# Kernel optimization log

Hardware: AMD Instinct MI355X
Metric: run time of the kernel (lower is better)

Reference implementation:

```python
import jax, jax.numpy as jnp
import numpy as np

B, H, K, D = 4096, 3, 32768, 128


def setup_inputs() -> dict:
    key = jax.random.key(0)
    k_in, k_emb = jax.random.split(key)
    inputs = jax.random.normal(k_in, (B, 1, D), dtype=jnp.float32)
    # xavier-uniform-ish init with per-head decay 0.5**h (gain 6.0), as in the module
    ks = jax.random.split(k_emb, H)
    tables = []
    for h in range(H):
        gain = 6.0 * (0.5 ** h)
        bound = gain * np.sqrt(6.0 / (K + D))
        tables.append(jax.random.uniform(ks[h], (K, D), jnp.float32, -bound, bound))
    emb = jnp.stack(tables, axis=0)  # [H, K, D]
    return {"inputs": inputs, "emb": emb}


def reference(inputs, emb):
    # Eval-mode HRQ forward: per-head negative squared-L2 distances to the
    # codebook on the running residual, hard argmax assignment, summed codes.
    x = inputs[:, 0, :]                      # [B, D]
    n_heads = emb.shape[0]
    resid = x
    quantized = jnp.zeros_like(x)
    codes = []
    for h in range(n_heads):
        W = emb[h]                            # [K, D]
        # -(||r||^2 + ||w||^2 - 2 r.w)  -> argmax == nearest code
        dists = -(jnp.sum(resid * resid, axis=1, keepdims=True)
                  + jnp.sum(W * W, axis=1)
                  - 2.0 * resid @ W.T)        # [B, K]
        c = jnp.argmax(dists, axis=-1)        # [B]
        q = jnp.take(W, c, axis=0)            # onehot(c) @ W == gather
        resid = resid - q
        quantized = quantized + q
        codes.append(c)
    loss = jnp.zeros(x.shape[0], dtype=inputs.dtype)
    return loss, quantized.reshape(inputs.shape), jnp.stack(codes, axis=1)
```

## Files before the change

### kernel.cpp

```cpp
#include <hip/hip_runtime.h>
#include <math.h>

#define NB 4096
#define NH 3
#define NK 32768
#define ND 128
#define KA 256
#define KB 256
#define RB 64
#define CS 16
#define CPB (NK / CS)
#define CI 128
#define NCI (CPB / CI)

typedef _Float16 half8_t __attribute__((ext_vector_type(8)));
typedef _Float16 half2_t __attribute__((ext_vector_type(2)));
typedef float f32x4 __attribute__((ext_vector_type(4)));
typedef __attribute__((address_space(1))) const unsigned int gu32_t;
typedef __attribute__((address_space(3))) unsigned int lu32_t;

__global__ __launch_bounds__(64) void init_kernel(const float* __restrict__ inp,
                                                  float* __restrict__ resid,
                                                  float* __restrict__ rr,
                                                  float* __restrict__ out,
                                                  _Float16* __restrict__ Aext) {
  int row = blockIdx.x;
  int lane = threadIdx.x;
  const float2* ip = (const float2*)(inp + row * ND);
  float2 v = ip[lane];
  ((float2*)(resid + row * ND))[lane] = v;
  ((float2*)(out + NB + row * ND))[lane] = make_float2(0.f, 0.f);
  if (lane == 0) out[row] = 0.f;
  _Float16 h0 = (_Float16)v.x, h1 = (_Float16)v.y;
  _Float16 l0 = (_Float16)(v.x - (float)h0), l1 = (_Float16)(v.y - (float)h1);
  half2_t h = {h0, h1}, l = {l0, l1};
  _Float16* base = Aext + (size_t)row * KA;
  *(half2_t*)(base + 2 * lane) = h;
  *(half2_t*)(base + 128 + 2 * lane) = l;
  float s = v.x * v.x + v.y * v.y;
  #pragma unroll
  for (int m = 32; m; m >>= 1) s += __shfl_xor(s, m, 64);
  if (lane == 0) rr[row] = s;
}

__global__ __launch_bounds__(256) void norms_kernel(const float* __restrict__ emb,
                                                    float* __restrict__ norms) {
  int row = blockIdx.x * 4 + (threadIdx.x >> 6);
  int lane = threadIdx.x & 63;
  const float2* wp = (const float2*)(emb + (size_t)row * ND);
  float2 v = wp[lane];
  float s = v.x * v.x + v.y * v.y;
  #pragma unroll
  for (int m = 32; m; m >>= 1) s += __shfl_xor(s, m, 64);
  if (lane == 0) norms[row] = s;
}

__global__ __launch_bounds__(256) void split_w_all_kernel(const float* __restrict__ emb,
                                                          _Float16* __restrict__ Bext) {
  const int head = blockIdx.x >> 11;
  const int cg = blockIdx.x & 2047;
  const int n_lo = threadIdx.x & 15;
  const int c = threadIdx.x >> 4;
  const int n = cg * 16 + n_lo;

  const float4* wp = (const float4*)(emb + (size_t)head * NK * ND + (size_t)n * ND + c * 8);
  float4 v0 = wp[0], v1 = wp[1];
  float xv[8] = {v0.x, v0.y, v0.z, v0.w, v1.x, v1.y, v1.z, v1.w};
  half8_t h, l;
  #pragma unroll
  for (int j = 0; j < 8; ++j) {
    _Float16 hh = (_Float16)xv[j];
    h[j] = hh;
    l[j] = (_Float16)(xv[j] - (float)hh);
  }
  const int ks0 = c >> 2;
  const int klo = c & 3;
  _Float16* base = Bext + (size_t)head * NK * KB + (size_t)(cg >> 2) * 16384 +
                   (cg & 3) * 512 + klo * 128 + n_lo * 8;
  *(half8_t*)(base + ks0 * 2048) = h;
  *(half8_t*)(base + (4 + ks0) * 2048) = l;
}

__global__ __launch_bounds__(256, 2) void score_mfma_kernel(
    const _Float16* __restrict__ Aext, const _Float16* __restrict__ Bext,
    const float* __restrict__ rr, const float* __restrict__ normh,
    float* __restrict__ partial_s, int* __restrict__ partial_i) {
  __shared__ __align__(16) _Float16 Ash[RB * KA];
  __shared__ __align__(16) float rrsh[RB];

  const int bid = blockIdx.x;
  const int cs = bid & (CS - 1);
  const int rowb = bid >> 4;
  const int rowBase = rowb * RB;
  const int colBase0 = cs * CPB;

  const int tid = threadIdx.x;
  const int lane = tid & 63;
  const int wn = tid >> 6;
  const int l15 = lane & 15;
  const int q = lane >> 4;

  {
    const int mrow = lane >> 3;
    const int cg = (lane & 7) ^ (mrow & 7);
    #pragma unroll
    for (int i = 0; i < 8; ++i) {
      int wc = wn * 8 + i;
      int p = wc >> 3;
      int m0 = (wc & 7) * 8;
      const _Float16* gA = Aext + (size_t)(rowBase + m0 + mrow) * KA + p * 64 + cg * 8;
      __builtin_amdgcn_global_load_lds((gu32_t*)gA, (lu32_t*)&Ash[(p * 64 + m0) * 64], 16, 0, 0);
    }
  }
  if (tid < RB) rrsh[tid] = rr[rowBase + tid];

  int aaddr0[4];
  #pragma unroll
  for (int mt = 0; mt < 4; ++mt) {
    int m = mt * 16 + l15;
    int slot = q ^ (m & 7);
    aaddr0[mt] = (m * 8 + slot) * 16;
  }

  float bs[16];
  int bi[16];
  #pragma unroll
  for (int t = 0; t < 16; ++t) { bs[t] = -INFINITY; bi[t] = 0x7fffffff; }

  unsigned bo = (unsigned)((colBase0 + (NCI - 1) * CI + wn * 32) >> 6) * 16384u +
                (((unsigned)(colBase0 + (NCI - 1) * CI + wn * 32) >> 4) & 3u) * 512u +
                (unsigned)lane * 8u;
  half8_t bh[2], bl[2];
  #pragma unroll
  for (int tn = 0; tn < 2; ++tn) {
    bh[tn] = *(const half8_t*)(Bext + bo + (unsigned)(tn * 512));
    bl[tn] = *(const half8_t*)(Bext + bo + (unsigned)(8192 + tn * 512));
  }

  __syncthreads();

  const f32x4 Z = {0.f, 0.f, 0.f, 0.f};

  #pragma unroll 1
  for (int ci = NCI - 1; ci >= 0; --ci) {
    const int ncol = colBase0 + ci * CI + wn * 32;
    const int ci_n = (ci > 0) ? ci - 1 : 0;
    const int ncol_n = colBase0 + ci_n * CI + wn * 32;
    const unsigned bon = (unsigned)(ncol_n >> 6) * 16384u +
                         (((unsigned)ncol_n >> 4) & 3u) * 512u + (unsigned)lane * 8u;

    float nw[2];
    #pragma unroll
    for (int tn = 0; tn < 2; ++tn) nw[tn] = normh[ncol + tn * 16 + l15];

    f32x4 acc[4][2];
    half8_t nh[2], nl[2];

    {
      #pragma unroll
      for (int tn = 0; tn < 2; ++tn) {
        nh[tn] = *(const half8_t*)(Bext + bo + (unsigned)(2048 + tn * 512));
        nl[tn] = *(const half8_t*)(Bext + bo + (unsigned)(2048 + 8192 + tn * 512));
      }
      __builtin_amdgcn_s_setprio(1);
      #pragma unroll
      for (int mt = 0; mt < 4; ++mt) {
        half8_t ah = *(const half8_t*)((const char*)Ash + aaddr0[mt]);
        half8_t al = *(const half8_t*)((const char*)Ash + aaddr0[mt] + 16384);
        acc[mt][0] = __builtin_amdgcn_mfma_f32_16x16x32_f16(ah, bh[0], Z, 0, 0, 0);
        acc[mt][1] = __builtin_amdgcn_mfma_f32_16x16x32_f16(ah, bh[1], Z, 0, 0, 0);
        acc[mt][0] = __builtin_amdgcn_mfma_f32_16x16x32_f16(al, bh[0], acc[mt][0], 0, 0, 0);
        acc[mt][1] = __builtin_amdgcn_mfma_f32_16x16x32_f16(al, bh[1], acc[mt][1], 0, 0, 0);
        acc[mt][0] = __builtin_amdgcn_mfma_f32_16x16x32_f16(ah, bl[0], acc[mt][0], 0, 0, 0);
        acc[mt][1] = __builtin_amdgcn_mfma_f32_16x16x32_f16(ah, bl[1], acc[mt][1], 0, 0, 0);
      }
      __builtin_amdgcn_s_setprio(0);
      bh[0] = nh[0]; bh[1] = nh[1];
      bl[0] = nl[0]; bl[1] = nl[1];
    }

    #pragma unroll
    for (int kc = 1; kc < 4; ++kc) {
      const unsigned po = (kc < 3) ? bo + (unsigned)((kc + 1) * 2048) : bon;
      #pragma unroll
      for (int tn = 0; tn < 2; ++tn) {
        nh[tn] = *(const half8_t*)(Bext + po + (unsigned)(tn * 512));
        nl[tn] = *(const half8_t*)(Bext + po + (unsigned)(8192 + tn * 512));
      }
      const int axor = (kc & 1) << 6;
      const int abase = (kc >> 1) * 8192;
      __builtin_amdgcn_s_setprio(1);
      #pragma unroll
      for (int mt = 0; mt < 4; ++mt) {
        half8_t ah = *(const half8_t*)((const char*)Ash + ((aaddr0[mt] ^ axor) + abase));
        half8_t al = *(const half8_t*)((const char*)Ash + ((aaddr0[mt] ^ axor) + abase + 16384));
        acc[mt][0] = __builtin_amdgcn_mfma_f32_16x16x32_f16(ah, bh[0], acc[mt][0], 0, 0, 0);
        acc[mt][1] = __builtin_amdgcn_mfma_f32_16x16x32_f16(ah, bh[1], acc[mt][1], 0, 0, 0);
        acc[mt][0] = __builtin_amdgcn_mfma_f32_16x16x32_f16(al, bh[0], acc[mt][0], 0, 0, 0);
        acc[mt][1] = __builtin_amdgcn_mfma_f32_16x16x32_f16(al, bh[1], acc[mt][1], 0, 0, 0);
        acc[mt][0] = __builtin_amdgcn_mfma_f32_16x16x32_f16(ah, bl[0], acc[mt][0], 0, 0, 0);
        acc[mt][1] = __builtin_amdgcn_mfma_f32_16x16x32_f16(ah, bl[1], acc[mt][1], 0, 0, 0);
      }
      __builtin_amdgcn_s_setprio(0);
      bh[0] = nh[0]; bh[1] = nh[1];
      bl[0] = nl[0]; bl[1] = nl[1];
    }

    #pragma unroll
    for (int tn = 1; tn >= 0; --tn) {
      const float nwv = nw[tn];
      const int cidx = ncol + tn * 16 + l15;
      #pragma unroll
      for (int mt = 0; mt < 4; ++mt) {
        const f32x4 rvv = *(const f32x4*)&rrsh[mt * 16 + q * 4];
        #pragma unroll
        for (int reg = 0; reg < 4; ++reg) {
          const int s = mt * 4 + reg;
          float t1 = rvv[reg] + nwv;
          float v = fmaf(2.0f, acc[mt][tn][reg], -t1);
          if (v >= bs[s]) { bs[s] = v; bi[s] = cidx; }
        }
      }
    }
    bo = bon;
  }

  __syncthreads();
  float* red_s = (float*)Ash;
  int* red_i = (int*)Ash + RB * 4;
  #pragma unroll
  for (int t = 0; t < 16; ++t) {
    float s = bs[t];
    int ii = bi[t];
    #pragma unroll
    for (int mask = 1; mask <= 8; mask <<= 1) {
      float os = __shfl_xor(s, mask, 64);
      int oi = __shfl_xor(ii, mask, 64);
      if (os > s || (os == s && oi < ii)) { s = os; ii = oi; }
    }
    if (l15 == 0) {
      int rloc = (t >> 2) * 16 + q * 4 + (t & 3);
      red_s[rloc * 4 + wn] = s;
      red_i[rloc * 4 + wn] = ii;
    }
  }
  __syncthreads();
  if (tid < RB) {
    float s0 = red_s[tid * 4];
    int i0 = red_i[tid * 4];
    #pragma unroll
    for (int x = 1; x < 4; ++x) {
      float sx = red_s[tid * 4 + x];
      int ix = red_i[tid * 4 + x];
      if (sx > s0 || (sx == s0 && ix < i0)) { s0 = sx; i0 = ix; }
    }
    partial_s[(size_t)(rowBase + tid) * CS + cs] = s0;
    partial_i[(size_t)(rowBase + tid) * CS + cs] = i0;
  }
}

__global__ __launch_bounds__(64) void reduce_update_kernel(const float* __restrict__ embh,
                                                           float* __restrict__ resid,
                                                           float* __restrict__ rr,
                                                           const float* __restrict__ ps,
                                                           const int* __restrict__ pi,
                                                           float* __restrict__ out,
                                                           _Float16* __restrict__ Aext, int h) {
  int row = blockIdx.x;
  int lane = threadIdx.x;
  float bs = -INFINITY;
  int bi = 0x7fffffff;
  if (lane < CS) {
    bs = ps[(size_t)row * CS + lane];
    bi = pi[(size_t)row * CS + lane];
  }
  #pragma unroll
  for (int m = 8; m; m >>= 1) {
    float os = __shfl_xor(bs, m, 64);
    int oi = __shfl_xor(bi, m, 64);
    if (os > bs || (os == bs && oi < bi)) { bs = os; bi = oi; }
  }
  int c = __shfl(bi, 0, 64);
  if (lane == 0) out[NB + NB * ND + row * NH + h] = (float)c;

  const float* wv = embh + (size_t)c * ND;
  float q0 = wv[lane], q1 = wv[lane + 64];
  float r0 = resid[row * ND + lane] - q0;
  float r1 = resid[row * ND + lane + 64] - q1;
  resid[row * ND + lane] = r0;
  resid[row * ND + lane + 64] = r1;
  out[NB + row * ND + lane] += q0;
  out[NB + row * ND + lane + 64] += q1;

  _Float16 h0 = (_Float16)r0, l0 = (_Float16)(r0 - (float)h0);
  _Float16 h1 = (_Float16)r1, l1 = (_Float16)(r1 - (float)h1);
  _Float16* ab = Aext + (size_t)row * KA;
  ab[lane] = h0;       ab[lane + 64] = h1;
  ab[128 + lane] = l0; ab[128 + lane + 64] = l1;

  float s = r0 * r0 + r1 * r1;
  #pragma unroll
  for (int m = 32; m; m >>= 1) s += __shfl_xor(s, m, 64);
  if (lane == 0) rr[row] = s;
}

extern "C" void kernel_launch(void* const* d_in, const int* in_sizes, int n_in,
                              void* d_out, int out_size, void* d_ws, size_t ws_size,
                              hipStream_t stream) {
  const float* inp = (const float*)d_in[0];
  const float* emb = (const float*)d_in[1];
  float* out = (float*)d_out;

  float* resid = (float*)d_ws;
  float* rr = resid + NB * ND;
  float* norms = rr + NB;
  float* ps = norms + NH * NK;
  int* pi = (int*)(ps + (size_t)NB * CS);
  _Float16* Aext = (_Float16*)(pi + (size_t)NB * CS);
  _Float16* Bext = Aext + (size_t)NB * KA;

  hipLaunchKernelGGL(init_kernel, dim3(NB), dim3(64), 0, stream, inp, resid, rr, out, Aext);
  hipLaunchKernelGGL(norms_kernel, dim3(NH * NK / 4), dim3(256), 0, stream, emb, norms);
  hipLaunchKernelGGL(split_w_all_kernel, dim3(NH * NK / 16), dim3(256), 0, stream, emb, Bext);
  for (int h = 0; h < NH; ++h) {
    hipLaunchKernelGGL(score_mfma_kernel, dim3((NB / RB) * CS), dim3(256), 0, stream,
                       Aext, Bext + (size_t)h * NK * KB, rr, norms + (size_t)h * NK, ps, pi);
    hipLaunchKernelGGL(reduce_update_kernel, dim3(NB), dim3(64), 0, stream,
                       emb + (size_t)h * NK * ND, resid, rr, ps, pi, out, Aext, h);
  }
}
```

Before: 423.2 us.

## Double row tile to 128 with 8 waves sharing B loads, pack argmax indices

Doubles the row block per workgroup to 128 and uses 8 waves (two row halves by four column groups), so each fetched B codebook tile is reused across twice as many rows and global B traffic is halved. The per-lane best-index registers are replaced by packed 8-bit chunk/tile tags that are decoded into column indices only at the end, which saves registers for the higher launch-bounds occupancy target. The risks are a larger LDS footprint, more register pressure under launch_bounds(512,4), and half as many workgroups.

```diff
diff --git a/kernel.cpp b/kernel.cpp
--- a/kernel.cpp
+++ b/kernel.cpp
@@ -7,7 +7,7 @@
 #define ND 128
 #define KA 256
 #define KB 256
-#define RB 64
+#define RB 128
 #define CS 16
 #define CPB (NK / CS)
 #define CI 128
@@ -81,7 +81,7 @@
   *(half8_t*)(base + (4 + ks0) * 2048) = l;
 }
 
-__global__ __launch_bounds__(256, 2) void score_mfma_kernel(
+__global__ __launch_bounds__(512, 4) void score_mfma_kernel(
     const _Float16* __restrict__ Aext, const _Float16* __restrict__ Bext,
     const float* __restrict__ rr, const float* __restrict__ normh,
     float* __restrict__ partial_s, int* __restrict__ partial_i) {
@@ -97,19 +97,21 @@
   const int tid = threadIdx.x;
   const int lane = tid & 63;
   const int wn = tid >> 6;
+  const int wc = wn & 3;
+  const int wr = wn >> 2;
   const int l15 = lane & 15;
   const int q = lane >> 4;
 
   {
+    const int p = wn >> 1;
+    const int mh = (wn & 1) * 64;
     const int mrow = lane >> 3;
     const int cg = (lane & 7) ^ (mrow & 7);
     #pragma unroll
     for (int i = 0; i < 8; ++i) {
-      int wc = wn * 8 + i;
-      int p = wc >> 3;
-      int m0 = (wc & 7) * 8;
+      const int m0 = mh + i * 8;
       const _Float16* gA = Aext + (size_t)(rowBase + m0 + mrow) * KA + p * 64 + cg * 8;
-      __builtin_amdgcn_global_load_lds((gu32_t*)gA, (lu32_t*)&Ash[(p * 64 + m0) * 64], 16, 0, 0);
+      __builtin_amdgcn_global_load_lds((gu32_t*)gA, (lu32_t*)&Ash[(p * 128 + m0) * 64], 16, 0, 0);
     }
   }
   if (tid < RB) rrsh[tid] = rr[rowBase + tid];
@@ -117,19 +119,24 @@
   int aaddr0[4];
   #pragma unroll
   for (int mt = 0; mt < 4; ++mt) {
-    int m = mt * 16 + l15;
-    int slot = q ^ (m & 7);
+    const int m = wr * 64 + mt * 16 + l15;
+    const int slot = q ^ (m & 7);
     aaddr0[mt] = (m * 8 + slot) * 16;
   }
 
   float bs[16];
-  int bi[16];
-  #pragma unroll
-  for (int t = 0; t < 16; ++t) { bs[t] = -INFINITY; bi[t] = 0x7fffffff; }
-
-  unsigned bo = (unsigned)((colBase0 + (NCI - 1) * CI + wn * 32) >> 6) * 16384u +
-                (((unsigned)(colBase0 + (NCI - 1) * CI + wn * 32) >> 4) & 3u) * 512u +
-                (unsigned)lane * 8u;
+  int pkb[4];
+  #pragma unroll
+  for (int t = 0; t < 16; ++t) bs[t] = -INFINITY;
+  #pragma unroll
+  for (int t = 0; t < 4; ++t) pkb[t] = 0;
+
+  unsigned bo;
+  {
+    const int ncol0 = colBase0 + (NCI - 1) * CI + wc * 32;
+    bo = (unsigned)(ncol0 >> 6) * 16384u + (((unsigned)ncol0 >> 4) & 3u) * 512u +
+         (unsigned)lane * 8u;
+  }
   half8_t bh[2], bl[2];
   #pragma unroll
   for (int tn = 0; tn < 2; ++tn) {
@@ -143,9 +150,9 @@
 
   #pragma unroll 1
   for (int ci = NCI - 1; ci >= 0; --ci) {
-    const int ncol = colBase0 + ci * CI + wn * 32;
+    const int ncol = colBase0 + ci * CI + wc * 32;
     const int ci_n = (ci > 0) ? ci - 1 : 0;
-    const int ncol_n = colBase0 + ci_n * CI + wn * 32;
+    const int ncol_n = colBase0 + ci_n * CI + wc * 32;
     const unsigned bon = (unsigned)(ncol_n >> 6) * 16384u +
                          (((unsigned)ncol_n >> 4) & 3u) * 512u + (unsigned)lane * 8u;
 
@@ -165,8 +172,9 @@
       __builtin_amdgcn_s_setprio(1);
       #pragma unroll
       for (int mt = 0; mt < 4; ++mt) {
-        half8_t ah = *(const half8_t*)((const char*)Ash + aaddr0[mt]);
-        half8_t al = *(const half8_t*)((const char*)Ash + aaddr0[mt] + 16384);
+        const char* ap = (const char*)Ash + aaddr0[mt];
+        half8_t ah = *(const half8_t*)ap;
+        half8_t al = *(const half8_t*)(ap + 32768);
         acc[mt][0] = __builtin_amdgcn_mfma_f32_16x16x32_f16(ah, bh[0], Z, 0, 0, 0);
         acc[mt][1] = __builtin_amdgcn_mfma_f32_16x16x32_f16(ah, bh[1], Z, 0, 0, 0);
         acc[mt][0] = __builtin_amdgcn_mfma_f32_16x16x32_f16(al, bh[0], acc[mt][0], 0, 0, 0);
@@ -188,12 +196,13 @@
         nl[tn] = *(const half8_t*)(Bext + po + (unsigned)(8192 + tn * 512));
       }
       const int axor = (kc & 1) << 6;
-      const int abase = (kc >> 1) * 8192;
+      const int abase = (kc >> 1) * 16384;
       __builtin_amdgcn_s_setprio(1);
       #pragma unroll
       for (int mt = 0; mt < 4; ++mt) {
-        half8_t ah = *(const half8_t*)((const char*)Ash + ((aaddr0[mt] ^ axor) + abase));
-        half8_t al = *(const half8_t*)((const char*)Ash + ((aaddr0[mt] ^ axor) + abase + 16384));
+        const char* ap = (const char*)Ash + ((aaddr0[mt] ^ axor) + abase);
+        half8_t ah = *(const half8_t*)ap;
+        half8_t al = *(const half8_t*)(ap + 32768);
         acc[mt][0] = __builtin_amdgcn_mfma_f32_16x16x32_f16(ah, bh[0], acc[mt][0], 0, 0, 0);
         acc[mt][1] = __builtin_amdgcn_mfma_f32_16x16x32_f16(ah, bh[1], acc[mt][1], 0, 0, 0);
         acc[mt][0] = __builtin_amdgcn_mfma_f32_16x16x32_f16(al, bh[0], acc[mt][0], 0, 0, 0);
@@ -209,16 +218,20 @@
     #pragma unroll
     for (int tn = 1; tn >= 0; --tn) {
       const float nwv = nw[tn];
-      const int cidx = ncol + tn * 16 + l15;
+      const int valb = (ci << 1) | tn;
       #pragma unroll
       for (int mt = 0; mt < 4; ++mt) {
-        const f32x4 rvv = *(const f32x4*)&rrsh[mt * 16 + q * 4];
+        const f32x4 rvv = *(const f32x4*)&rrsh[wr * 64 + mt * 16 + q * 4];
         #pragma unroll
         for (int reg = 0; reg < 4; ++reg) {
           const int s = mt * 4 + reg;
           float t1 = rvv[reg] + nwv;
           float v = fmaf(2.0f, acc[mt][tn][reg], -t1);
-          if (v >= bs[s]) { bs[s] = v; bi[s] = cidx; }
+          bool u = (v >= bs[s]);
+          bs[s] = u ? v : bs[s];
+          const int sh = (s & 3) * 8;
+          int upd = (pkb[s >> 2] & ~(0xFF << sh)) | (valb << sh);
+          pkb[s >> 2] = u ? upd : pkb[s >> 2];
         }
       }
     }
@@ -228,10 +241,12 @@
   __syncthreads();
   float* red_s = (float*)Ash;
   int* red_i = (int*)Ash + RB * 4;
+  const int cb = colBase0 + wc * 32 + l15;
   #pragma unroll
   for (int t = 0; t < 16; ++t) {
     float s = bs[t];
-    int ii = bi[t];
+    const int vb = (pkb[t >> 2] >> ((t & 3) * 8)) & 0xFF;
+    int ii = cb + (vb >> 1) * CI + (vb & 1) * 16;
     #pragma unroll
     for (int mask = 1; mask <= 8; mask <<= 1) {
       float os = __shfl_xor(s, mask, 64);
@@ -239,9 +254,9 @@
       if (os > s || (os == s && oi < ii)) { s = os; ii = oi; }
     }
     if (l15 == 0) {
-      int rloc = (t >> 2) * 16 + q * 4 + (t & 3);
-      red_s[rloc * 4 + wn] = s;
-      red_i[rloc * 4 + wn] = ii;
+      const int rloc = wr * 64 + (t >> 2) * 16 + q * 4 + (t & 3);
+      red_s[rloc * 4 + wc] = s;
+      red_i[rloc * 4 + wc] = ii;
     }
   }
   __syncthreads();
@@ -323,7 +338,7 @@
   hipLaunchKernelGGL(norms_kernel, dim3(NH * NK / 4), dim3(256), 0, stream, emb, norms);
   hipLaunchKernelGGL(split_w_all_kernel, dim3(NH * NK / 16), dim3(256), 0, stream, emb, Bext);
   for (int h = 0; h < NH; ++h) {
-    hipLaunchKernelGGL(score_mfma_kernel, dim3((NB / RB) * CS), dim3(256), 0, stream,
+    hipLaunchKernelGGL(score_mfma_kernel, dim3((NB / RB) * CS), dim3(512), 0, stream,
                        Aext, Bext + (size_t)h * NK * KB, rr, norms + (size_t)h * NK, ps, pi);
     hipLaunchKernelGGL(reduce_update_kernel, dim3(NB), dim3(64), 0, stream,
                        emb + (size_t)h * NK * ND, resid, rr, ps, pi, out, Aext, h);
```

Result: slower. 1.102 ms (+160.5%).
